# Kernel optimization log

Measured on AMD Instinct MI355X. Metric: run time of the kernel, lower is better.

Reference implementation:

```python
import jax, jax.numpy as jnp
import numpy as np

EPS = 1e-6
BETA = 0.25
COMMIT_W = 1.0


def setup_inputs() -> dict:
    key = jax.random.key(0)
    k1, k2, k3 = jax.random.split(key, 3)
    b, c, h, w = 8, 256, 32, 32
    n_e, e_dim = 16384, 256
    z = jax.random.normal(k1, (b, c, h, w), jnp.float32)
    # frozen_codebook = randn(n_e, e_dim) * e_dim**-0.5
    codebook = jax.random.normal(k2, (n_e, e_dim), jnp.float32) * (e_dim ** -0.5)
    # nn.Linear(e_dim, in_channels, bias=False) weight: (in_channels, e_dim)
    W = jax.random.normal(k3, (c, e_dim), jnp.float32) * (e_dim ** -0.5)
    return {"z": z, "codebook": codebook, "W": W}


def _rotate_to(src, tgt):
    # Rotation trick (Fifty et al.): rotate src onto tgt direction with a
    # detached Householder-style transform; gradient flows through src only.
    # src, tgt: (n, d)
    norm_src = jnp.linalg.norm(src, axis=-1, keepdims=True)
    norm_tgt = jnp.linalg.norm(tgt, axis=-1, keepdims=True)
    u = src / (norm_src + EPS)
    q = tgt / (norm_tgt + EPS)
    uq = u + q
    w_ = jax.lax.stop_gradient(uq / (jnp.linalg.norm(uq, axis=-1, keepdims=True) + EPS))
    u_d = jax.lax.stop_gradient(u)
    q_d = jax.lax.stop_gradient(q)
    rot = (src
           - 2.0 * jnp.sum(src * w_, axis=-1, keepdims=True) * w_
           + 2.0 * jnp.sum(src * u_d, axis=-1, keepdims=True) * q_d)
    return rot * jax.lax.stop_gradient(norm_tgt / (norm_src + EPS))


def reference(z, codebook, W):
    b, c, h, w = z.shape
    # b c h w -> (b*h*w, c)
    z_flat = jnp.transpose(z, (0, 2, 3, 1)).reshape(-1, c)
    # implicit codebook: frozen codes through linear projection
    emb = codebook @ W.T  # (n_e, c)
    # squared L2 distances (no grad needed for argmin)
    d = (jnp.sum(z_flat ** 2, axis=1, keepdims=True)
         + jnp.sum(emb ** 2, axis=1)
         - 2.0 * (z_flat @ emb.T))  # (n_tok, n_e)
    indices = jnp.argmin(d, axis=1)  # (n_tok,)
    z_q_flat = emb[indices]  # gather quantized vectors
    loss = COMMIT_W * (jnp.mean((jax.lax.stop_gradient(z_flat) - z_q_flat) ** 2)
                       + BETA * jnp.mean((z_flat - jax.lax.stop_gradient(z_q_flat)) ** 2))
    z_q_flat = _rotate_to(z_flat, z_q_flat)
    z_q = jnp.transpose(z_q_flat.reshape(b, h, w, c), (0, 3, 1, 2))
    return z_q, loss, indices
```

## Files before the change

### kernel.cpp

```cpp
#include <hip/hip_runtime.h>
#include <math.h>

#define EPSV 1e-6f
#define NTOK 8192
#define NE   16384
#define DIM  256

using short8 = __attribute__((ext_vector_type(8))) short;
using f32x4v = __attribute__((ext_vector_type(4))) float;

__device__ __forceinline__ unsigned short f2bf(float v) {
    unsigned int u = __float_as_uint(v);
    u += 0x7fffu + ((u >> 16) & 1u);
    return (unsigned short)(u >> 16);
}
__device__ __forceinline__ float bf2f(unsigned short h) {
    return __uint_as_float(((unsigned int)h) << 16);
}

__device__ __forceinline__ void gload_lds16(const void* g, void* s) {
    __builtin_amdgcn_global_load_lds(
        (const __attribute__((address_space(1))) void*)g,
        (__attribute__((address_space(3))) void*)s, 16, 0, 0);
}

__device__ __forceinline__ void split8(const float4 a, const float4 b,
                                       short8& h, short8& l) {
    float f[8] = {a.x, a.y, a.z, a.w, b.x, b.y, b.z, b.w};
#pragma unroll
    for (int j = 0; j < 8; ++j) {
        unsigned short hh = f2bf(f[j]);
        h[j] = (short)hh;
        l[j] = (short)f2bf(f[j] - bf2f(hh));
    }
}

__global__ __launch_bounds__(256) void f1_pre(
    const float* __restrict__ zin, float* __restrict__ z_flat,
    unsigned short* __restrict__ zh, unsigned short* __restrict__ zl,
    float* __restrict__ sz, const float* __restrict__ Wm,
    unsigned short* __restrict__ wh, unsigned short* __restrict__ wl) {
    const int bid = blockIdx.x;
    const int tid = threadIdx.x;
    if (bid >= 128) {
        const int i = ((bid - 128) * 256 + tid) * 4;
        const float4 v = *(const float4*)(Wm + i);
        float f[4] = {v.x, v.y, v.z, v.w};
#pragma unroll
        for (int j = 0; j < 4; ++j) {
            unsigned short h = f2bf(f[j]);
            wh[i + j] = h;
            wl[i + j] = f2bf(f[j] - bf2f(h));
        }
        return;
    }
    __shared__ float tile[64][65];
    const int yx0 = (bid & 15) * 64, b = bid >> 4;
    const int sub = tid >> 6, ln = tid & 63;
    double dacc[16];
#pragma unroll
    for (int j = 0; j < 16; ++j) dacc[j] = 0.0;

    for (int cc = 0; cc < 4; ++cc) {
        const int c0 = cc * 64;
        __syncthreads();
#pragma unroll
        for (int j = 0; j < 16; ++j) {
            int cl = j * 4 + sub;
            tile[cl][ln] = zin[((size_t)(b * 256 + c0 + cl) << 10) + yx0 + ln];
        }
        __syncthreads();
#pragma unroll
        for (int j = 0; j < 16; ++j) {
            int tl = j * 4 + sub;
            float v = tile[ln][tl];
            size_t o = (size_t)(b * 1024 + yx0 + tl) * 256 + c0 + ln;
            z_flat[o] = v;
            unsigned short h = f2bf(v);
            zh[o] = h;
            zl[o] = f2bf(v - bf2f(h));
            dacc[j] += (double)v * v;
        }
    }
#pragma unroll
    for (int j = 0; j < 16; ++j) {
        double s = dacc[j];
#pragma unroll
        for (int m = 1; m < 64; m <<= 1) s += __shfl_xor(s, m);
        if (ln == 0) sz[b * 1024 + yx0 + j * 4 + sub] = (float)s;
    }
}

__global__ __launch_bounds__(256, 2) void k0c_emb(
    const float* __restrict__ cb, const unsigned short* __restrict__ wh,
    const unsigned short* __restrict__ wl, float* __restrict__ emb,
    unsigned short* __restrict__ eh, unsigned short* __restrict__ el,
    float* __restrict__ se0, float* __restrict__ se1) {
    __shared__ char smemC[65536];
    const int tid = threadIdx.x;
    const int w = tid >> 6, lane = tid & 63;
    const int quad = lane >> 4, lr = lane & 15;
    const int wr = w & 1, wc = w >> 1;
    const int n0 = blockIdx.x * 128, c0 = blockIdx.y * 128;

    f32x4v acc[4][4];
#pragma unroll
    for (int mt = 0; mt < 4; ++mt)
#pragma unroll
        for (int nt = 0; nt < 4; ++nt)
            acc[mt][nt] = (f32x4v){0.f, 0.f, 0.f, 0.f};

    for (int kc = 0; kc < 4; ++kc) {
        __syncthreads();
#pragma unroll
        for (int i = 0; i < 16; ++i) {
            int s = i * 4 + w;
            int u = s * 64 + lane;
            const void* g;
            if (s < 32) {
                int kg = u >> 7, row = u & 127;
                g = cb + (size_t)(n0 + row) * 256 + kc * 64 + kg * 4;
            } else if (s < 48) {
                int u1 = u - 2048;
                int kg = u1 >> 7, row = u1 & 127;
                g = wh + (size_t)(c0 + row) * 256 + kc * 64 + kg * 8;
            } else {
                int u2 = u - 3072;
                int kg = u2 >> 7, row = u2 & 127;
                g = wl + (size_t)(c0 + row) * 256 + kc * 64 + kg * 8;
            }
            gload_lds16(g, smemC + ((size_t)u << 4));
        }
        __syncthreads();
#pragma unroll
        for (int ks = 0; ks < 2; ++ks) {
            short8 Ah[4], Al[4], Bh[4], Bl[4];
#pragma unroll
            for (int mt = 0; mt < 4; ++mt) {
                int m = wr * 64 + mt * 16 + lr;
                int kg2 = ks * 8 + quad * 2;
                float4 f0 = *(const float4*)(smemC + (((size_t)kg2 * 128 + m) << 4));
                float4 f1 = *(const float4*)(smemC + ((((size_t)kg2 + 1) * 128 + m) << 4));
                split8(f0, f1, Ah[mt], Al[mt]);
            }
#pragma unroll
            for (int nt = 0; nt < 4; ++nt) {
                int n = wc * 64 + nt * 16 + lr;
                int ku = (ks * 4 + quad) * 128 + n;
                Bh[nt] = *(const short8*)(smemC + (((size_t)2048 + ku) << 4));
                Bl[nt] = *(const short8*)(smemC + (((size_t)3072 + ku) << 4));
            }
#pragma unroll
            for (int mt = 0; mt < 4; ++mt)
#pragma unroll
                for (int nt = 0; nt < 4; ++nt) {
                    f32x4v a = acc[mt][nt];
                    a = __builtin_amdgcn_mfma_f32_16x16x32_bf16(Ah[mt], Bh[nt], a, 0, 0, 0);
                    a = __builtin_amdgcn_mfma_f32_16x16x32_bf16(Ah[mt], Bl[nt], a, 0, 0, 0);
                    a = __builtin_amdgcn_mfma_f32_16x16x32_bf16(Al[mt], Bh[nt], a, 0, 0, 0);
                    a = __builtin_amdgcn_mfma_f32_16x16x32_bf16(Al[mt], Bl[nt], a, 0, 0, 0);
                    acc[mt][nt] = a;
                }
        }
    }
#pragma unroll
    for (int mt = 0; mt < 4; ++mt)
#pragma unroll
        for (int rr = 0; rr < 4; ++rr) {
            int row = n0 + wr * 64 + mt * 16 + quad * 4 + rr;
#pragma unroll
            for (int nt = 0; nt < 4; ++nt) {
                int col = c0 + wc * 64 + nt * 16 + lr;
                size_t o = (size_t)row * 256 + col;
                float v = acc[mt][nt][rr];
                emb[o] = v;
                unsigned short h = f2bf(v);
                eh[o] = h;
                el[o] = f2bf(v - bf2f(h));
            }
        }
    __syncthreads();
    float* sblk = (float*)smemC;
#pragma unroll
    for (int mt = 0; mt < 4; ++mt)
#pragma unroll
        for (int rr = 0; rr < 4; ++rr) {
            float s = 0.f;
#pragma unroll
            for (int nt = 0; nt < 4; ++nt) {
                float v = acc[mt][nt][rr];
                s = fmaf(v, v, s);
            }
#pragma unroll
            for (int st = 1; st < 16; st <<= 1) s += __shfl_xor(s, st);
            if (lr == 0)
                sblk[wc * 128 + wr * 64 + mt * 16 + quad * 4 + rr] = s;
        }
    __syncthreads();
    if (tid < 128) {
        float* sep = (blockIdx.y == 0) ? se0 : se1;
        sep[n0 + tid] = sblk[tid] + sblk[128 + tid];
    }
}

__global__ __launch_bounds__(256, 4) void k1_dist_argmin(
    const unsigned short* __restrict__ zh, const unsigned short* __restrict__ zl,
    const unsigned short* __restrict__ eh, const unsigned short* __restrict__ el,
    const float* __restrict__ sz, const float* __restrict__ se0,
    const float* __restrict__ se1, float* __restrict__ pval,
    int* __restrict__ pidx) {
    __shared__ short8 smem[2][1024];
    const int tid = threadIdx.x;
    const int w = tid >> 6, lane = tid & 63;
    const int quad = lane >> 4, lr = lane & 15;
    const int bid = blockIdx.x;
    const int slab = bid & 7;
    const int rowBase = (bid >> 3) * 64 + w * 16;
    const int slabBase = slab * 2048;

    short8 Ah[8], Al[8];
#pragma unroll
    for (int ks = 0; ks < 8; ++ks) {
        size_t o = (size_t)(rowBase + lr) * 256 + ks * 32 + quad * 8;
        Ah[ks] = *(const short8*)(zh + o);
        Al[ks] = *(const short8*)(zl + o);
    }

    float szr[4];
#pragma unroll
    for (int rr = 0; rr < 4; ++rr)
        szr[rr] = sz[rowBase + quad * 4 + rr];

    float minv[4];
    int mini[4];
#pragma unroll
    for (int rr = 0; rr < 4; ++rr) {
        minv[rr] = INFINITY;
        mini[rr] = 0;
    }

    auto stage = [&](int buf, int ch) {
        const int colBase = slabBase + ch * 16;
#pragma unroll
        for (int i = 0; i < 4; ++i) {
            int u = i * 256 + tid;
            int fmt = u >> 9;
            int u1 = u & 511;
            int col = u1 >> 5, kgs = u1 & 31;
            int kg = kgs ^ col;
            const unsigned short* g =
                (fmt ? el : eh) + (size_t)(colBase + col) * 256 + kg * 8;
            gload_lds16(g, (char*)&smem[0][0] + buf * 16384 +
                               (((size_t)i * 256 + w * 64) << 4));
        }
    };

    stage(0, 0);
    __syncthreads();

    for (int ch = 0; ch < 128; ++ch) {
        const int cur = ch & 1;
        if (ch + 1 < 128) stage(cur ^ 1, ch + 1);

        const int colg = slabBase + ch * 16 + lr;
        const float sec = se0[colg] + se1[colg];

        f32x4v acc = (f32x4v){0.f, 0.f, 0.f, 0.f};

#pragma unroll
        for (int ks = 0; ks < 8; ++ks) {
            const int kgs = (ks * 4 + quad) ^ lr;
            short8 Bh = smem[cur][lr * 32 + kgs];
            short8 Bl = smem[cur][512 + lr * 32 + kgs];
            acc = __builtin_amdgcn_mfma_f32_16x16x32_bf16(Ah[ks], Bh, acc, 0, 0, 0);
            acc = __builtin_amdgcn_mfma_f32_16x16x32_bf16(Ah[ks], Bl, acc, 0, 0, 0);
            acc = __builtin_amdgcn_mfma_f32_16x16x32_bf16(Al[ks], Bh, acc, 0, 0, 0);
        }

#pragma unroll
        for (int rr = 0; rr < 4; ++rr) {
            float szse = __fadd_rn(szr[rr], sec);
            float d = fmaf(-2.0f, acc[rr], szse);
            if (d < minv[rr]) {
                minv[rr] = d;
                mini[rr] = colg;
            }
        }
        __syncthreads();
    }

#pragma unroll
    for (int st = 1; st < 16; st <<= 1) {
#pragma unroll
        for (int rr = 0; rr < 4; ++rr) {
            float ov = __shfl_xor(minv[rr], st);
            int oi = __shfl_xor(mini[rr], st);
            if (ov < minv[rr] ||
                (ov == minv[rr] && oi < mini[rr])) {
                minv[rr] = ov;
                mini[rr] = oi;
            }
        }
    }
    if (lr == 0) {
#pragma unroll
        for (int rr = 0; rr < 4; ++rr) {
            int row = rowBase + quad * 4 + rr;
            pval[(size_t)row * 8 + slab] = minv[rr];
            pidx[(size_t)row * 8 + slab] = mini[rr];
        }
    }
}

__global__ __launch_bounds__(256) void k3a_token(
    const float* __restrict__ z_flat, const float* __restrict__ emb,
    const float* __restrict__ pval, const int* __restrict__ pidx,
    float* __restrict__ alpha, float* __restrict__ beta,
    int* __restrict__ idxf, float* __restrict__ out,
    float* __restrict__ lpart) {
    __shared__ float red[4];
    const int w = threadIdx.x >> 6, lane = threadIdx.x & 63;
    const int t = blockIdx.x * 4 + w;

    float bv = INFINITY;
    int bi = 0x7fffffff;
    if (lane < 8) {
        bv = pval[(size_t)t * 8 + lane];
        bi = pidx[(size_t)t * 8 + lane];
    }
#pragma unroll
    for (int st = 1; st < 8; st <<= 1) {
        float ov = __shfl_xor(bv, st);
        int oi = __shfl_xor(bi, st);
        if (ov < bv || (ov == bv && oi < bi)) { bv = ov; bi = oi; }
    }
    const int best = __shfl(bi, 0);

    const float4 zv = *(const float4*)(z_flat + (size_t)t * 256 + lane * 4);
    const float4 ev = *(const float4*)(emb + (size_t)best * 256 + lane * 4);
    float szs = zv.x * zv.x + zv.y * zv.y + zv.z * zv.z + zv.w * zv.w;
    float ses = ev.x * ev.x + ev.y * ev.y + ev.z * ev.z + ev.w * ev.w;
    float zes = zv.x * ev.x + zv.y * ev.y + zv.z * ev.z + zv.w * ev.w;
    float dx = zv.x - ev.x, dy = zv.y - ev.y, dz = zv.z - ev.z, dw = zv.w - ev.w;
    float sqs = dx * dx + dy * dy + dz * dz + dw * dw;
#pragma unroll
    for (int m = 1; m < 64; m <<= 1) {
        szs += __shfl_xor(szs, m);
        ses += __shfl_xor(ses, m);
        zes += __shfl_xor(zes, m);
        sqs += __shfl_xor(sqs, m);
    }
    if (lane == 0) {
        float ns = sqrtf(szs), nt = sqrtf(ses);
        float inv_s = 1.0f / (ns + EPSV);
        float inv_t = 1.0f / (nt + EPSV);
        float s2 = szs * inv_s;
        float su = szs * inv_s * inv_s;
        float sq = ses * inv_t * inv_t;
        float uq = zes * inv_s * inv_t;
        float nw = sqrtf(su + sq + 2.0f * uq);
        float inv_w = 1.0f / (nw + EPSV);
        float s1 = (s2 + zes * inv_t) * inv_w;
        float scale = nt * inv_s;
        float a = scale * (1.0f - 2.0f * s1 * inv_w * inv_s);
        float bb = scale * inv_t * 2.0f * (s2 - s1 * inv_w);
        alpha[t] = a;
        beta[t] = bb;
        idxf[t] = best;
        out[2097153 + t] = (float)best;
        red[w] = sqs;
    }
    __syncthreads();
    if (threadIdx.x == 0)
        lpart[blockIdx.x] = red[0] + red[1] + red[2] + red[3];
}

__global__ __launch_bounds__(256) void k3b_zq(
    const float* __restrict__ zin, const float* __restrict__ emb,
    const float* __restrict__ alpha, const float* __restrict__ beta,
    const int* __restrict__ idxf, const float* __restrict__ lpart,
    float* __restrict__ out) {
    if (blockIdx.x == 0) {
        __shared__ float red[4];
        const int tid = threadIdx.x;
        float s = 0.0f;
        for (int i = tid; i < 2048; i += 256) s += lpart[i];
#pragma unroll
        for (int m = 1; m < 64; m <<= 1) s += __shfl_xor(s, m);
        if ((tid & 63) == 0) red[tid >> 6] = s;
        __syncthreads();
        if (tid == 0)
            out[2097152] = 1.25f * (red[0] + red[1] + red[2] + red[3]) *
                           (1.0f / 2097152.0f);
    }
    const int i = blockIdx.x * 256 + threadIdx.x;
    const int c = (i >> 10) & 255;
    const int t = ((i >> 18) << 10) | (i & 1023);
    out[i] = alpha[t] * zin[i] + beta[t] * emb[(size_t)idxf[t] * 256 + c];
}

extern "C" void kernel_launch(void* const* d_in, const int* in_sizes, int n_in,
                              void* d_out, int out_size, void* d_ws,
                              size_t ws_size, hipStream_t stream) {
    (void)in_sizes; (void)n_in; (void)out_size; (void)ws_size;
    const float* zin = (const float*)d_in[0];
    const float* cb  = (const float*)d_in[1];
    const float* Wm  = (const float*)d_in[2];
    float* out = (float*)d_out;
    char* ws = (char*)d_ws;

    float*          z_flat = (float*)(ws + 0);
    unsigned short* zh     = (unsigned short*)(ws + 8388608);
    unsigned short* zl     = (unsigned short*)(ws + 12582912);
    float*          emb    = (float*)(ws + 16777216);
    unsigned short* eh     = (unsigned short*)(ws + 33554432);
    unsigned short* el     = (unsigned short*)(ws + 41943040);
    float*          sz     = (float*)(ws + 50331648);
    float*          se0    = (float*)(ws + 50364416);
    float*          se1    = (float*)(ws + 50429952);
    float*          pval   = (float*)(ws + 50495488);
    int*            pidx   = (int*)(ws + 50757632);
    float*          alpha  = (float*)(ws + 51019776);
    float*          beta   = (float*)(ws + 51052544);
    int*            idxf   = (int*)(ws + 51085312);
    float*          lpart  = (float*)(ws + 51118080);
    unsigned short* wh     = (unsigned short*)(ws + 51126272);
    unsigned short* wl     = (unsigned short*)(ws + 51257344);

    f1_pre<<<192, 256, 0, stream>>>(zin, z_flat, zh, zl, sz, Wm, wh, wl);
    k0c_emb<<<dim3(128, 2), 256, 0, stream>>>(cb, wh, wl, emb, eh, el,
                                              se0, se1);
    k1_dist_argmin<<<1024, 256, 0, stream>>>(zh, zl, eh, el, sz,
                                             se0, se1, pval, pidx);
    k3a_token<<<2048, 256, 0, stream>>>(z_flat, emb, pval, pidx, alpha, beta,
                                        idxf, out, lpart);
    k3b_zq<<<8192, 256, 0, stream>>>(zin, emb, alpha, beta, idxf, lpart, out);
}
```

Measured before the change: 301.6 us.

## Retile distance-argmin kernel to 512 threads with 32-column chunks

```diff
diff --git a/kernel.cpp b/kernel.cpp
--- a/kernel.cpp
+++ b/kernel.cpp
@@ -203,20 +203,24 @@
     }
 }
 
-__global__ __launch_bounds__(256, 4) void k1_dist_argmin(
+__global__ __launch_bounds__(512, 4) void k1_dist_argmin(
     const unsigned short* __restrict__ zh, const unsigned short* __restrict__ zl,
     const unsigned short* __restrict__ eh, const unsigned short* __restrict__ el,
     const float* __restrict__ sz, const float* __restrict__ se0,
     const float* __restrict__ se1, float* __restrict__ pval,
     int* __restrict__ pidx) {
-    __shared__ short8 smem[2][1024];
+    __shared__ short8 smem[2][2048];
+    __shared__ float seS[2048];
     const int tid = threadIdx.x;
     const int w = tid >> 6, lane = tid & 63;
     const int quad = lane >> 4, lr = lane & 15;
     const int bid = blockIdx.x;
     const int slab = bid & 7;
-    const int rowBase = (bid >> 3) * 64 + w * 16;
+    const int rowBase = (bid >> 3) * 128 + w * 16;
     const int slabBase = slab * 2048;
+
+    for (int j = tid; j < 2048; j += 512)
+        seS[j] = __fadd_rn(se0[slabBase + j], se1[slabBase + j]);
 
     short8 Ah[8], Al[8];
 #pragma unroll
@@ -239,53 +243,78 @@
         mini[rr] = 0;
     }
 
+    const unsigned short* gp[4];
+#pragma unroll
+    for (int i = 0; i < 4; ++i) {
+        int u = i * 512 + tid;
+        int fmt = u >> 10;
+        int u1 = u & 1023;
+        int col = u1 >> 5, kgs = u1 & 31;
+        int kg = kgs ^ col;
+        gp[i] = (fmt ? el : eh) + (size_t)(slabBase + col) * 256 + kg * 8;
+    }
+
     auto stage = [&](int buf, int ch) {
-        const int colBase = slabBase + ch * 16;
+        const int off = ch << 13;
 #pragma unroll
         for (int i = 0; i < 4; ++i) {
-            int u = i * 256 + tid;
-            int fmt = u >> 9;
-            int u1 = u & 511;
-            int col = u1 >> 5, kgs = u1 & 31;
-            int kg = kgs ^ col;
-            const unsigned short* g =
-                (fmt ? el : eh) + (size_t)(colBase + col) * 256 + kg * 8;
-            gload_lds16(g, (char*)&smem[0][0] + buf * 16384 +
-                               (((size_t)i * 256 + w * 64) << 4));
+            gload_lds16(gp[i] + off, (char*)&smem[0][0] + buf * 32768 +
+                                         (((size_t)i * 512 + w * 64) << 4));
+        }
+    };
+
+    auto compute_ep = [&](int cur, int ch) {
+        f32x4v acc0 = (f32x4v){0.f, 0.f, 0.f, 0.f};
+        f32x4v acc1 = (f32x4v){0.f, 0.f, 0.f, 0.f};
+        const int col0 = lr, col1 = 16 + lr;
+#pragma unroll
+        for (int ks = 0; ks < 8; ++ks) {
+            const int kq = ks * 4 + quad;
+            const int k0 = kq ^ col0, k1i = kq ^ col1;
+            short8 Bh0 = smem[cur][col0 * 32 + k0];
+            short8 Bl0 = smem[cur][1024 + col0 * 32 + k0];
+            short8 Bh1 = smem[cur][col1 * 32 + k1i];
+            short8 Bl1 = smem[cur][1024 + col1 * 32 + k1i];
+            acc0 = __builtin_amdgcn_mfma_f32_16x16x32_bf16(Ah[ks], Bh0, acc0, 0, 0, 0);
+            acc1 = __builtin_amdgcn_mfma_f32_16x16x32_bf16(Ah[ks], Bh1, acc1, 0, 0, 0);
+            acc0 = __builtin_amdgcn_mfma_f32_16x16x32_bf16(Ah[ks], Bl0, acc0, 0, 0, 0);
+            acc1 = __builtin_amdgcn_mfma_f32_16x16x32_bf16(Ah[ks], Bl1, acc1, 0, 0, 0);
+            acc0 = __builtin_amdgcn_mfma_f32_16x16x32_bf16(Al[ks], Bh0, acc0, 0, 0, 0);
+            acc1 = __builtin_amdgcn_mfma_f32_16x16x32_bf16(Al[ks], Bh1, acc1, 0, 0, 0);
+        }
+        const int base = ch * 32;
+        {
+            const int colg = slabBase + base + lr;
+            const float sec = seS[base + lr];
+#pragma unroll
+            for (int rr = 0; rr < 4; ++rr) {
+                float szse = __fadd_rn(szr[rr], sec);
+                float d = fmaf(-2.0f, acc0[rr], szse);
+                if (d < minv[rr]) { minv[rr] = d; mini[rr] = colg; }
+            }
+        }
+        {
+            const int colg = slabBase + base + 16 + lr;
+            const float sec = seS[base + 16 + lr];
+#pragma unroll
+            for (int rr = 0; rr < 4; ++rr) {
+                float szse = __fadd_rn(szr[rr], sec);
+                float d = fmaf(-2.0f, acc1[rr], szse);
+                if (d < minv[rr]) { minv[rr] = d; mini[rr] = colg; }
+            }
         }
     };
 
     stage(0, 0);
     __syncthreads();
 
-    for (int ch = 0; ch < 128; ++ch) {
-        const int cur = ch & 1;
-        if (ch + 1 < 128) stage(cur ^ 1, ch + 1);
-
-        const int colg = slabBase + ch * 16 + lr;
-        const float sec = se0[colg] + se1[colg];
-
-        f32x4v acc = (f32x4v){0.f, 0.f, 0.f, 0.f};
-
-#pragma unroll
-        for (int ks = 0; ks < 8; ++ks) {
-            const int kgs = (ks * 4 + quad) ^ lr;
-            short8 Bh = smem[cur][lr * 32 + kgs];
-            short8 Bl = smem[cur][512 + lr * 32 + kgs];
-            acc = __builtin_amdgcn_mfma_f32_16x16x32_bf16(Ah[ks], Bh, acc, 0, 0, 0);
-            acc = __builtin_amdgcn_mfma_f32_16x16x32_bf16(Ah[ks], Bl, acc, 0, 0, 0);
-            acc = __builtin_amdgcn_mfma_f32_16x16x32_bf16(Al[ks], Bh, acc, 0, 0, 0);
-        }
-
-#pragma unroll
-        for (int rr = 0; rr < 4; ++rr) {
-            float szse = __fadd_rn(szr[rr], sec);
-            float d = fmaf(-2.0f, acc[rr], szse);
-            if (d < minv[rr]) {
-                minv[rr] = d;
-                mini[rr] = colg;
-            }
-        }
+#pragma unroll 1
+    for (int ch = 0; ch < 64; ch += 2) {
+        stage(1, ch + 1);
+        compute_ep(0, ch);
+        __syncthreads();
+        if (ch + 2 < 64) stage(0, ch + 2);
+        compute_ep(1, ch + 1);
         __syncthreads();
     }
 
@@ -430,8 +459,8 @@
     f1_pre<<<192, 256, 0, stream>>>(zin, z_flat, zh, zl, sz, Wm, wh, wl);
     k0c_emb<<<dim3(128, 2), 256, 0, stream>>>(cb, wh, wl, emb, eh, el,
                                               se0, se1);
-    k1_dist_argmin<<<1024, 256, 0, stream>>>(zh, zl, eh, el, sz,
-                                             se0, se1, pval, pidx);
+    k1_dist_argmin<<<512, 512, 0, stream>>>(zh, zl, eh, el, sz,
+                                            se0, se1, pval, pidx);
     k3a_token<<<2048, 256, 0, stream>>>(z_flat, emb, pval, pidx, alpha, beta,
                                         idxf, out, lpart);
     k3b_zq<<<8192, 256, 0, stream>>>(zin, emb, alpha, beta, idxf, lpart, out);
```

After: 304.4 us. No clear change (+0.9%).
